# Kernel tuning notes

Measured on AMD Instinct MI355X. Metric: run time of the kernel, lower is better.

The kernel has to match this reference:

```python
import jax, jax.numpy as jnp
import numpy as np

B_, L_, D_, R_, N_ = 8, 1024, 512, 32, 16  # batch, seq(in_channels), dim(=dim_inner), dt_rank, d_state


def setup_inputs() -> dict:
    key = jax.random.key(0)
    ks = jax.random.split(key, 8)
    s = lambda k, shape, scale: jax.random.normal(k, shape, dtype=jnp.float32) * scale
    inv = D_ ** -0.5
    return {
        "x": jax.random.uniform(ks[0], (B_, L_, D_), dtype=jnp.float32),
        "W1": s(ks[1], (D_, D_), inv), "b1": jnp.zeros((D_,), jnp.float32),
        "W2": s(ks[2], (D_, D_), inv), "b2": jnp.zeros((D_,), jnp.float32),
        "Wout": s(ks[3], (D_, D_), inv), "bout": jnp.zeros((D_,), jnp.float32),
        "conv_w": s(ks[4], (L_, L_, 3), (3 * L_) ** -0.5),  # Conv1d(L_, L_, k=3) weight (O,I,W)
        "conv_b": jnp.zeros((L_,), jnp.float32),
        "W_dbc": s(ks[5], (R_ + 2 * N_, D_), inv),          # deltaBC projection (no bias)
        "W_dt": s(ks[6], (D_, R_), R_ ** -0.5),             # dt_proj weight
        "b_dt": jnp.zeros((D_,), jnp.float32),
        "A_log": jnp.log(jnp.tile(jnp.arange(1, N_ + 1, dtype=jnp.float32), (D_, 1))),  # (D, N)
        "Dp": jnp.ones((D_,), jnp.float32),
    }


def _silu(v):
    return v * jax.nn.sigmoid(v)


def _selective_scan(u, delta, A, Bm, Cm, Dp):
    # u, delta: (b, l, d); A: (d, n); Bm, Cm: (b, l, n); Dp: (d,)
    dA = jnp.exp(jnp.einsum('bld,dn->bldn', delta, A))          # (b,l,d,n)
    dBu = jnp.einsum('bld,bln,bld->bldn', delta, Bm, u)          # (b,l,d,n)

    def step(h, inp):
        dA_t, dBu_t, C_t = inp                                   # (b,d,n),(b,d,n),(b,n)
        h = dA_t * h + dBu_t
        return h, jnp.einsum('bdn,bn->bd', h, C_t)

    h0 = jnp.zeros((u.shape[0], u.shape[2], A.shape[1]), u.dtype)
    _, ys = jax.lax.scan(step, h0, (dA.transpose(1, 0, 2, 3), dBu.transpose(1, 0, 2, 3), Cm.transpose(1, 0, 2)))
    return ys.transpose(1, 0, 2) + u * Dp                        # (b,l,d)


def reference(x, W1, b1, W2, b2, Wout, bout, conv_w, conv_b, W_dbc, W_dt, b_dt, A_log, Dp):
    skip = x
    x1 = x @ W1.T + b1                                            # proj_one
    x2 = x @ W2.T + b2                                            # proj_two
    # Conv1d over channel axis = L_ (dim 1), spatial axis = D_ (dim 2)
    x1 = jax.lax.conv_general_dilated(x1, conv_w, window_strides=(1,), padding=((1, 1),),
                                      dimension_numbers=('NCW', 'OIW', 'NCW')) + conv_b[None, :, None]
    x1 = _silu(x1)
    # SSM (zeta-style): deltaBC -> split -> dt_proj -> softplus -> selective scan
    dbc = x1 @ W_dbc.T                                            # (b,l,R+2N)
    delta = jax.nn.softplus(dbc[..., :R_] @ W_dt.T + b_dt)        # (b,l,d)
    Bm, Cm = dbc[..., R_:R_ + N_], dbc[..., R_ + N_:]
    A = -jnp.exp(A_log)
    y = _selective_scan(x1, delta, A, Bm, Cm, Dp)
    out = y * _silu(x2) + skip
    return out @ Wout.T + bout
```

## Files before the change

### kernel.cpp

```cpp
#include <hip/hip_runtime.h>
#include <hip/hip_bf16.h>
#include <hip/hip_fp16.h>

typedef __hip_bfloat16 bf16;
typedef __bf16 bf16x8 __attribute__((ext_vector_type(8)));
typedef float f32x4 __attribute__((ext_vector_type(4)));

static_assert(sizeof(bf16) == 2, "bf16 must be 2 bytes");

#define NC 32
#define CH 32
#define X1TP_BSTRIDE (514L * 1024)

__device__ __forceinline__ float silu_f(float v) { return v / (1.0f + __expf(-v)); }

__device__ __forceinline__ void gload16(const bf16* g, bf16* l) {
  __builtin_amdgcn_global_load_lds((const __attribute__((address_space(1))) void*)g,
                                   (__attribute__((address_space(3))) void*)l,
                                   16, 0, 0);
}

template <int N> __device__ __forceinline__ void wait_vm() {
  static_assert(N == 0 || N == 4 || N == 6 || N == 8 || N == 12, "add case");
  if constexpr (N == 0)       asm volatile("s_waitcnt vmcnt(0)" ::: "memory");
  else if constexpr (N == 4)  asm volatile("s_waitcnt vmcnt(4)" ::: "memory");
  else if constexpr (N == 6)  asm volatile("s_waitcnt vmcnt(6)" ::: "memory");
  else if constexpr (N == 8)  asm volatile("s_waitcnt vmcnt(8)" ::: "memory");
  else if constexpr (N == 12) asm volatile("s_waitcnt vmcnt(12)" ::: "memory");
}

__global__ __launch_bounds__(256) void prep_all(
    const float* __restrict__ x, const float* __restrict__ W1,
    const float* __restrict__ W2, const float* __restrict__ Wout,
    const float* __restrict__ Wdbc, const float* __restrict__ convw,
    bf16* __restrict__ xb, bf16* __restrict__ w1b, bf16* __restrict__ w2b,
    bf16* __restrict__ woutb, bf16* __restrict__ wdbcb,
    bf16* __restrict__ cws, bf16* __restrict__ x1tp) {
  const int gid = blockIdx.x * 256 + threadIdx.x;
  auto cvt4 = [](const float* src, bf16* dst, long q) {
    float4 v = *reinterpret_cast<const float4*>(src + q * 4);
    ushort4 s;
    s.x = __builtin_bit_cast(unsigned short, __float2bfloat16(v.x));
    s.y = __builtin_bit_cast(unsigned short, __float2bfloat16(v.y));
    s.z = __builtin_bit_cast(unsigned short, __float2bfloat16(v.z));
    s.w = __builtin_bit_cast(unsigned short, __float2bfloat16(v.w));
    *reinterpret_cast<ushort4*>(dst + q * 4) = s;
  };
  if (gid < 1048576) {
    cvt4(x, xb, gid);
  } else if (gid < 1114112) {
    cvt4(W1, w1b, gid - 1048576);
  } else if (gid < 1179648) {
    cvt4(W2, w2b, gid - 1114112);
  } else if (gid < 1245184) {
    cvt4(Wout, woutb, gid - 1179648);
  } else if (gid < 1253376) {
    cvt4(Wdbc, wdbcb, gid - 1245184);
  } else if (gid < 2301952) {
    long idx = gid - 1253376;
    int o = (int)(idx >> 10), i = (int)(idx & 1023);
    float a = convw[idx * 3], b = convw[idx * 3 + 1], c = convw[idx * 3 + 2];
    cws[(long)o * 3072 + i]        = __float2bfloat16(a);
    cws[(long)o * 3072 + 1024 + i] = __float2bfloat16(b);
    cws[(long)o * 3072 + 2048 + i] = __float2bfloat16(c);
  } else {
    int e = gid - 2301952;
    int b = e >> 11, rem = e & 2047;
    int r = rem >> 10, ii = rem & 1023;
    x1tp[(long)b * X1TP_BSTRIDE + (long)r * (513 * 1024) + ii] = __float2bfloat16(0.f);
  }
}

template <int EPI, int BM, int BN, int CONVB, int NBUF>
__device__ __forceinline__ void gemm_body(const bf16* __restrict__ A,
                                          const bf16* __restrict__ Bw,
                                          const float* __restrict__ bias,
                                          float* __restrict__ outf,
                                          bf16* __restrict__ outb,
                                          int M, int N, int K, int lda, int ldb,
                                          long sAz, long sBz, long sOz,
                                          int bx, int by, int z,
                                          bf16* As, bf16* Bs) {
  constexpr int BK = 64;
  constexpr int MI = BM / 32, WNF = BN / 32;
  constexpr int APW = BM / 32, BPW = BN / 32;
  constexpr int IPW = APW + BPW;

  const int tid = threadIdx.x;
  const int w = tid >> 6, l = tid & 63;
  const int wm = w >> 1, wn = w & 1;
  const int m0 = bx * BM, n0 = by * BN;
  const bf16* Ab = A + (long)z * sAz + (long)m0 * lda;
  const bf16* Bb = Bw + (long)z * sBz;

  const int lrow = l >> 3;
  const int lcol = (((l & 7) ^ (l >> 3)) << 3);

  auto stage = [&](int buf, int k0) {
#pragma unroll
    for (int j = 0; j < APW; ++j) {
      int iss = w * APW + j;
      int row = iss * 8 + lrow;
      gload16(Ab + (long)row * lda + k0 + lcol, &As[buf * BM * 64 + iss * 512]);
    }
#pragma unroll
    for (int j = 0; j < BPW; ++j) {
      int iss = w * BPW + j;
      int row = iss * 8 + lrow;
      const bf16* src;
      if (CONVB) src = Bb + (long)(n0 + row + (k0 >> 10)) * 1024 + (k0 & 1023) + lcol;
      else       src = Bb + (long)(n0 + row) * ldb + k0 + lcol;
      gload16(src, &Bs[buf * BN * 64 + iss * 512]);
    }
  };

  f32x4 acc[MI][WNF] = {};
  const int nt = K / BK;
  const int lr = l & 15;
  const int lko = (l >> 4) * 8;
  const int xorm = (lr & 7) << 3;

#pragma unroll
  for (int s = 0; s < NBUF - 1; ++s) stage(s, s * BK);
  for (int t = 0; t < nt; ++t) {
    const int cur = t % NBUF;
    if (t + NBUF - 1 < nt) {
      stage((t + NBUF - 1) % NBUF, (t + NBUF - 1) * BK);
      wait_vm<(NBUF - 1) * IPW>();
    } else {
      wait_vm<0>();
    }
    __builtin_amdgcn_s_barrier();
    __builtin_amdgcn_sched_barrier(0);
#pragma unroll
    for (int kk = 0; kk < 2; ++kk) {
      const int col = (lko + kk * 32) ^ xorm;
      bf16x8 af[MI], bfg[WNF];
#pragma unroll
      for (int mi = 0; mi < MI; ++mi)
        af[mi] = *reinterpret_cast<const bf16x8*>(
            &As[cur * BM * 64 + (wm * (BM / 2) + mi * 16 + lr) * 64 + col]);
#pragma unroll
      for (int ni = 0; ni < WNF; ++ni)
        bfg[ni] = *reinterpret_cast<const bf16x8*>(
            &Bs[cur * BN * 64 + (wn * (BN / 2) + ni * 16 + lr) * 64 + col]);
#pragma unroll
      for (int mi = 0; mi < MI; ++mi)
#pragma unroll
        for (int ni = 0; ni < WNF; ++ni)
          acc[mi][ni] = __builtin_amdgcn_mfma_f32_16x16x32_bf16(af[mi], bfg[ni], acc[mi][ni], 0, 0, 0);
    }
    __builtin_amdgcn_sched_barrier(0);
    __builtin_amdgcn_s_barrier();
  }

  const int lq = l >> 4;
#pragma unroll
  for (int mi = 0; mi < MI; ++mi) {
#pragma unroll
    for (int ni = 0; ni < WNF; ++ni) {
#pragma unroll
      for (int j = 0; j < 4; ++j) {
        int m = m0 + wm * (BM / 2) + mi * 16 + lq * 4 + j;
        int n = n0 + wn * (BN / 2) + ni * 16 + lr;
        float v = acc[mi][ni][j];
        if (EPI == 2) {
          v += bias[m];
          (outb + (long)z * sOz)[(long)m * N + n] = __float2bfloat16(silu_f(v));
        } else if (EPI == 3) {
          outf[(long)m * N + n] = v;
        } else if (EPI == 4) {
          v += bias[n];
          outf[(long)m * N + n] = v;
        } else if (EPI == 5) {
          v += bias[m];
          int b = n >> 10, li = n & 1023;
          outb[(long)b * X1TP_BSTRIDE + (long)(m + 1) * 1024 + li] = __float2bfloat16(v);
        } else {
          v += bias[n];
          outb[(long)m * N + n] = __float2bfloat16(silu_f(v));
        }
      }
    }
  }
}

template <int EPI, int BM, int BN, int CONVB, int NBUF, int GX, int GY>
__global__ __launch_bounds__(256) void gemm_nt(const bf16* __restrict__ A,
                                               const bf16* __restrict__ Bw,
                                               const float* __restrict__ bias,
                                               float* __restrict__ outf,
                                               bf16* __restrict__ outb,
                                               int M, int N, int K, int lda, int ldb,
                                               long sAz, long sBz, long sOz) {
  __shared__ __align__(16) bf16 As[NBUF * BM * 64];
  __shared__ __align__(16) bf16 Bs[NBUF * BN * 64];
  const int bid = (blockIdx.x & 7) * ((int)gridDim.x >> 3) + (blockIdx.x >> 3);
  const int by = bid % GY;
  const int bx = (bid / GY) % GX;
  const int z  = bid / (GX * GY);
  gemm_body<EPI, BM, BN, CONVB, NBUF>(A, Bw, bias, outf, outb, M, N, K, lda, ldb,
                                      sAz, sBz, sOz, bx, by, z, As, Bs);
}

__global__ __launch_bounds__(256) void gemm_dual(
    const bf16* __restrict__ w1b, const bf16* __restrict__ xb1,
    const float* __restrict__ b1, bf16* __restrict__ x1tp,
    const bf16* __restrict__ xb2, const bf16* __restrict__ w2b,
    const float* __restrict__ b2, bf16* __restrict__ x2g) {
  __shared__ __align__(16) bf16 As[2 * 128 * 64];
  __shared__ __align__(16) bf16 Bs[2 * 128 * 64];
  int bid = (blockIdx.x & 7) * 64 + (blockIdx.x >> 3);
  if (bid < 256) {
    int by = bid & 63, bx = bid >> 6;
    gemm_body<5, 128, 128, 0, 2>(w1b, xb1, b1, nullptr, x1tp, 512, 8192, 512, 512, 512,
                                 0, 0, 0, bx, by, 0, As, Bs);
  } else {
    bid -= 256;
    int by = bid & 3, bx = bid >> 2;
    gemm_body<6, 128, 128, 0, 2>(xb2, w2b, b2, nullptr, x2g, 8192, 512, 512, 512, 512,
                                 0, 0, 0, bx, by, 0, As, Bs);
  }
}

__global__ __launch_bounds__(256) void delta_kernel(const float* __restrict__ dbc,
                                                    const float* __restrict__ W_dt,
                                                    const float* __restrict__ b_dt,
                                                    __half* __restrict__ delta) {
  const int tid = threadIdx.x;
  const int d = blockIdx.x * 256 + tid;
  const int r0 = blockIdx.y * 8;
  __shared__ float sD[8][32];
  {
    int tt = tid >> 5, j = tid & 31;
    sD[tt][j] = dbc[(long)(r0 + tt) * 64 + j];
  }
  __syncthreads();
  float wdt[32];
#pragma unroll
  for (int r = 0; r < 32; r += 4) {
    float4 v = *reinterpret_cast<const float4*>(&W_dt[(long)d * 32 + r]);
    wdt[r] = v.x; wdt[r + 1] = v.y; wdt[r + 2] = v.z; wdt[r + 3] = v.w;
  }
  const float bd = b_dt[d];
#pragma unroll
  for (int tt = 0; tt < 8; ++tt) {
    float a = bd;
#pragma unroll
    for (int r = 0; r < 32; ++r) a = fmaf(sD[tt][r], wdt[r], a);
    delta[(long)(r0 + tt) * 512 + d] = __float2half(fmaxf(a, 0.f) + log1pf(__expf(-fabsf(a))));
  }
}

__global__ __launch_bounds__(256) void scan_p1(const bf16* __restrict__ u_bf,
                                               const float* __restrict__ dbc,
                                               const __half* __restrict__ delta,
                                               const float* __restrict__ A_log,
                                               __half* __restrict__ P,
                                               __half* __restrict__ Q) {
  const int tid = threadIdx.x;
  const int nh = tid & 1;
  const int d = blockIdx.x * 128 + (tid >> 1);
  const int c = blockIdx.y, b = blockIdx.z;
  __shared__ float sB[CH][16];
  for (int i = tid; i < CH * 16; i += 256) {
    int tt = i >> 4, j = i & 15;
    sB[tt][j] = dbc[((long)b * 1024 + c * CH + tt) * 64 + 32 + j];
  }
  __syncthreads();
  float Adn[8];
#pragma unroll
  for (int n = 0; n < 8; ++n) Adn[n] = -__expf(A_log[d * 16 + nh * 8 + n]);
  float p[8], q[8];
#pragma unroll
  for (int n = 0; n < 8; ++n) { p[n] = 1.f; q[n] = 0.f; }
  const long rowb = (long)b * 1024 + c * CH;
  for (int tt = 0; tt < CH; ++tt) {
    long off = (rowb + tt) * 512 + d;
    float dv = __half2float(delta[off]);
    float uv = __bfloat162float(u_bf[off]);
    float s = dv * uv;
#pragma unroll
    for (int n = 0; n < 8; ++n) {
      float dA = __expf(dv * Adn[n]);
      p[n] *= dA;
      q[n] = fmaf(dA, q[n], s * sB[tt][nh * 8 + n]);
    }
  }
  __half* Pp = P + ((long)b * NC + c) * 8192 + (long)d * 16 + nh * 8;
  __half* Qp = Q + ((long)b * NC + c) * 8192 + (long)d * 16 + nh * 8;
  __half tp[8], tq[8];
#pragma unroll
  for (int n = 0; n < 8; ++n) { tp[n] = __float2half(p[n]); tq[n] = __float2half(q[n]); }
  *reinterpret_cast<uint4*>(Pp) = *reinterpret_cast<uint4*>(tp);
  *reinterpret_cast<uint4*>(Qp) = *reinterpret_cast<uint4*>(tq);
}

__global__ __launch_bounds__(256) void scan_p2(const __half* __restrict__ P,
                                               const __half* __restrict__ Q,
                                               __half* __restrict__ Hin) {
  const int dn = blockIdx.x * 256 + threadIdx.x;
  const int b = blockIdx.y;
  float h = 0.f;
#pragma unroll 4
  for (int c = 0; c < NC; ++c) {
    long idx = ((long)b * NC + c) * 8192 + dn;
    Hin[idx] = __float2half(h);
    h = fmaf(__half2float(P[idx]), h, __half2float(Q[idx]));
  }
}

__global__ __launch_bounds__(256) void scan_p3(const bf16* __restrict__ u_bf,
                                               const float* __restrict__ dbc,
                                               const __half* __restrict__ delta,
                                               const float* __restrict__ A_log,
                                               const float* __restrict__ Dp,
                                               const bf16* __restrict__ x2g,
                                               const bf16* __restrict__ xres,
                                               const __half* __restrict__ Hin,
                                               bf16* __restrict__ zb) {
  const int tid = threadIdx.x;
  const int nh = tid & 1;
  const int d = blockIdx.x * 128 + (tid >> 1);
  const int c = blockIdx.y, b = blockIdx.z;
  __shared__ float sBC[CH][32];
  for (int i = tid; i < CH * 32; i += 256) {
    int tt = i >> 5, j = i & 31;
    sBC[tt][j] = dbc[((long)b * 1024 + c * CH + tt) * 64 + 32 + j];
  }
  __syncthreads();
  float Adn[8];
#pragma unroll
  for (int n = 0; n < 8; ++n) Adn[n] = -__expf(A_log[d * 16 + nh * 8 + n]);
  float h[8];
  {
    const __half* Hp = Hin + ((long)b * NC + c) * 8192 + (long)d * 16 + nh * 8;
    __half th[8];
    *reinterpret_cast<uint4*>(th) = *reinterpret_cast<const uint4*>(Hp);
#pragma unroll
    for (int n = 0; n < 8; ++n) h[n] = __half2float(th[n]);
  }
  const float Dpv = Dp[d];
  const long rowb = (long)b * 1024 + c * CH;
  for (int tt = 0; tt < CH; ++tt) {
    long off = (rowb + tt) * 512 + d;
    float dv = __half2float(delta[off]);
    float uv = __bfloat162float(u_bf[off]);
    float s = dv * uv;
    float y = nh ? 0.f : uv * Dpv;
#pragma unroll
    for (int n = 0; n < 8; ++n) {
      float dA = __expf(dv * Adn[n]);
      h[n] = fmaf(dA, h[n], s * sBC[tt][nh * 8 + n]);
      y = fmaf(h[n], sBC[tt][16 + nh * 8 + n], y);
    }
    y += __shfl_xor(y, 1);
    if (nh == 0) {
      float gate = __bfloat162float(x2g[off]);
      float xv = __bfloat162float(xres[off]);
      zb[off] = __float2bfloat16(fmaf(y, gate, xv));
    }
  }
}

extern "C" void kernel_launch(void* const* d_in, const int* in_sizes, int n_in,
                              void* d_out, int out_size, void* d_ws, size_t ws_size,
                              hipStream_t stream) {
  (void)in_sizes; (void)n_in; (void)out_size; (void)ws_size;
  const float* x    = (const float*)d_in[0];
  const float* W1   = (const float*)d_in[1];
  const float* b1   = (const float*)d_in[2];
  const float* W2   = (const float*)d_in[3];
  const float* b2   = (const float*)d_in[4];
  const float* Wout = (const float*)d_in[5];
  const float* bout = (const float*)d_in[6];
  const float* convw = (const float*)d_in[7];
  const float* convb = (const float*)d_in[8];
  const float* Wdbc = (const float*)d_in[9];
  const float* Wdt  = (const float*)d_in[10];
  const float* bdt  = (const float*)d_in[11];
  const float* Alog = (const float*)d_in[12];
  const float* Dp   = (const float*)d_in[13];
  float* out = (float*)d_out;

  char* ws = (char*)d_ws;
  size_t off = 0;
  auto alloc = [&](size_t bytes) { void* p = ws + off; off += (bytes + 255) & ~(size_t)255; return p; };
  bf16* xb      = (bf16*)alloc(8192L * 512 * 2);
  bf16* w1b     = (bf16*)alloc(512L * 512 * 2);
  bf16* w2b     = (bf16*)alloc(512L * 512 * 2);
  bf16* woutb   = (bf16*)alloc(512L * 512 * 2);
  bf16* wdbcb   = (bf16*)alloc(64L * 512 * 2);
  bf16* cws     = (bf16*)alloc(1024L * 3072 * 2);
  bf16* x1tp    = (bf16*)alloc(8L * X1TP_BSTRIDE * 2);
  bf16* x2g     = (bf16*)alloc(8192L * 512 * 2);
  bf16* x1s     = (bf16*)alloc(8192L * 512 * 2);
  float* dbc    = (float*)alloc(8192L * 64 * 4);
  __half* delta = (__half*)alloc(8192L * 512 * 2);
  __half* P     = (__half*)alloc(8L * NC * 8192 * 2);
  __half* Q     = (__half*)alloc(8L * NC * 8192 * 2);
  __half* Hin   = (__half*)alloc(8L * NC * 8192 * 2);
  bf16* zb = xb;

  prep_all<<<9056, 256, 0, stream>>>(x, W1, W2, Wout, Wdbc, convw,
                                     xb, w1b, w2b, woutb, wdbcb, cws, x1tp);
  gemm_dual<<<512, 256, 0, stream>>>(w1b, xb, b1, x1tp, xb, w2b, b2, x2g);
  gemm_nt<2, 64, 128, 1, 3, 16, 4><<<512, 256, 0, stream>>>(
      cws, x1tp, convb, nullptr, x1s, 1024, 512, 3072, 3072, 0,
      0, X1TP_BSTRIDE, 1024L * 512);
  gemm_nt<3, 64, 64, 0, 3, 128, 1><<<128, 256, 0, stream>>>(
      x1s, wdbcb, nullptr, dbc, nullptr, 8192, 64, 512, 512, 512, 0, 0, 0);
  delta_kernel<<<dim3(2, 1024), 256, 0, stream>>>(dbc, Wdt, bdt, delta);
  scan_p1<<<dim3(4, NC, 8), 256, 0, stream>>>(x1s, dbc, delta, Alog, P, Q);
  scan_p2<<<dim3(32, 8, 1), 256, 0, stream>>>(P, Q, Hin);
  scan_p3<<<dim3(4, NC, 8), 256, 0, stream>>>(x1s, dbc, delta, Alog, Dp, x2g, xb, Hin, zb);
  gemm_nt<4, 64, 128, 0, 3, 128, 4><<<512, 256, 0, stream>>>(
      zb, woutb, bout, out, nullptr, 8192, 512, 512, 512, 512, 0, 0, 0);
}
```

Before: 163.9 us.

## Fuse dt projection and softplus into scan kernels, drop delta buffer

Removes the standalone delta_kernel and computes delta = softplus(dbc[:R] @ W_dt^T + b_dt) per chunk inside both scan_p1 and scan_p3, storing it in shared memory. This eliminates one kernel launch and the write and two reads of an 8 MB fp16 delta tensor. In exchange, the 32-wide dot product and softplus are computed twice, once in each scan pass, and shared memory per block grows. Delta now stays in fp32 instead of being rounded to fp16.

```diff
diff --git a/kernel.cpp b/kernel.cpp
--- a/kernel.cpp
+++ b/kernel.cpp
@@ -223,51 +223,47 @@
   }
 }
 
-__global__ __launch_bounds__(256) void delta_kernel(const float* __restrict__ dbc,
-                                                    const float* __restrict__ W_dt,
-                                                    const float* __restrict__ b_dt,
-                                                    __half* __restrict__ delta) {
-  const int tid = threadIdx.x;
-  const int d = blockIdx.x * 256 + tid;
-  const int r0 = blockIdx.y * 8;
-  __shared__ float sD[8][32];
-  {
-    int tt = tid >> 5, j = tid & 31;
-    sD[tt][j] = dbc[(long)(r0 + tt) * 64 + j];
-  }
-  __syncthreads();
-  float wdt[32];
-#pragma unroll
-  for (int r = 0; r < 32; r += 4) {
-    float4 v = *reinterpret_cast<const float4*>(&W_dt[(long)d * 32 + r]);
-    wdt[r] = v.x; wdt[r + 1] = v.y; wdt[r + 2] = v.z; wdt[r + 3] = v.w;
-  }
-  const float bd = b_dt[d];
-#pragma unroll
-  for (int tt = 0; tt < 8; ++tt) {
-    float a = bd;
-#pragma unroll
-    for (int r = 0; r < 32; ++r) a = fmaf(sD[tt][r], wdt[r], a);
-    delta[(long)(r0 + tt) * 512 + d] = __float2half(fmaxf(a, 0.f) + log1pf(__expf(-fabsf(a))));
-  }
-}
-
 __global__ __launch_bounds__(256) void scan_p1(const bf16* __restrict__ u_bf,
                                                const float* __restrict__ dbc,
-                                               const __half* __restrict__ delta,
+                                               const float* __restrict__ W_dt,
+                                               const float* __restrict__ b_dt,
                                                const float* __restrict__ A_log,
                                                __half* __restrict__ P,
                                                __half* __restrict__ Q) {
   const int tid = threadIdx.x;
+  const int c = blockIdx.y, b = blockIdx.z;
+  __shared__ float sD[CH][64];
+  __shared__ float sDel[CH][128];
+  for (int i = tid; i < CH * 16; i += 256) {
+    int tt = i >> 4, j4 = i & 15;
+    *reinterpret_cast<float4*>(&sD[tt][j4 * 4]) =
+        *reinterpret_cast<const float4*>(&dbc[((long)b * 1024 + c * CH + tt) * 64 + j4 * 4]);
+  }
+  __syncthreads();
+  {
+    const int d_loc = tid & 127, th = tid >> 7;
+    const int dg = blockIdx.x * 128 + d_loc;
+    float wdt[32];
+#pragma unroll
+    for (int r = 0; r < 32; r += 4) {
+      float4 v = *reinterpret_cast<const float4*>(&W_dt[(long)dg * 32 + r]);
+      wdt[r] = v.x; wdt[r + 1] = v.y; wdt[r + 2] = v.z; wdt[r + 3] = v.w;
+    }
+    const float bd = b_dt[dg];
+#pragma unroll
+    for (int k = 0; k < 16; ++k) {
+      int tt = th * 16 + k;
+      float a = bd;
+#pragma unroll
+      for (int r = 0; r < 32; ++r) a = fmaf(sD[tt][r], wdt[r], a);
+      sDel[tt][d_loc] = fmaxf(a, 0.f) + log1pf(__expf(-fabsf(a)));
+    }
+  }
+  __syncthreads();
+
   const int nh = tid & 1;
-  const int d = blockIdx.x * 128 + (tid >> 1);
-  const int c = blockIdx.y, b = blockIdx.z;
-  __shared__ float sB[CH][16];
-  for (int i = tid; i < CH * 16; i += 256) {
-    int tt = i >> 4, j = i & 15;
-    sB[tt][j] = dbc[((long)b * 1024 + c * CH + tt) * 64 + 32 + j];
-  }
-  __syncthreads();
+  const int dl = tid >> 1;
+  const int d = blockIdx.x * 128 + dl;
   float Adn[8];
 #pragma unroll
   for (int n = 0; n < 8; ++n) Adn[n] = -__expf(A_log[d * 16 + nh * 8 + n]);
@@ -276,15 +272,14 @@
   for (int n = 0; n < 8; ++n) { p[n] = 1.f; q[n] = 0.f; }
   const long rowb = (long)b * 1024 + c * CH;
   for (int tt = 0; tt < CH; ++tt) {
-    long off = (rowb + tt) * 512 + d;
-    float dv = __half2float(delta[off]);
-    float uv = __bfloat162float(u_bf[off]);
+    float dv = sDel[tt][dl];
+    float uv = __bfloat162float(u_bf[(rowb + tt) * 512 + d]);
     float s = dv * uv;
 #pragma unroll
     for (int n = 0; n < 8; ++n) {
       float dA = __expf(dv * Adn[n]);
       p[n] *= dA;
-      q[n] = fmaf(dA, q[n], s * sB[tt][nh * 8 + n]);
+      q[n] = fmaf(dA, q[n], s * sD[tt][32 + nh * 8 + n]);
     }
   }
   __half* Pp = P + ((long)b * NC + c) * 8192 + (long)d * 16 + nh * 8;
@@ -312,7 +307,8 @@
 
 __global__ __launch_bounds__(256) void scan_p3(const bf16* __restrict__ u_bf,
                                                const float* __restrict__ dbc,
-                                               const __half* __restrict__ delta,
+                                               const float* __restrict__ W_dt,
+                                               const float* __restrict__ b_dt,
                                                const float* __restrict__ A_log,
                                                const float* __restrict__ Dp,
                                                const bf16* __restrict__ x2g,
@@ -320,39 +316,63 @@
                                                const __half* __restrict__ Hin,
                                                bf16* __restrict__ zb) {
   const int tid = threadIdx.x;
+  const int c = blockIdx.y, b = blockIdx.z;
+  __shared__ float sD[CH][64];
+  __shared__ float sDel[CH][128];
+  for (int i = tid; i < CH * 16; i += 256) {
+    int tt = i >> 4, j4 = i & 15;
+    *reinterpret_cast<float4*>(&sD[tt][j4 * 4]) =
+        *reinterpret_cast<const float4*>(&dbc[((long)b * 1024 + c * CH + tt) * 64 + j4 * 4]);
+  }
+  __syncthreads();
+  {
+    const int d_loc = tid & 127, th = tid >> 7;
+    const int dg = blockIdx.x * 128 + d_loc;
+    float wdt[32];
+#pragma unroll
+    for (int r = 0; r < 32; r += 4) {
+      float4 v = *reinterpret_cast<const float4*>(&W_dt[(long)dg * 32 + r]);
+      wdt[r] = v.x; wdt[r + 1] = v.y; wdt[r + 2] = v.z; wdt[r + 3] = v.w;
+    }
+    const float bd = b_dt[dg];
+#pragma unroll
+    for (int k = 0; k < 16; ++k) {
+      int tt = th * 16 + k;
+      float a = bd;
+#pragma unroll
+      for (int r = 0; r < 32; ++r) a = fmaf(sD[tt][r], wdt[r], a);
+      sDel[tt][d_loc] = fmaxf(a, 0.f) + log1pf(__expf(-fabsf(a)));
+    }
+  }
+  __syncthreads();
+
   const int nh = tid & 1;
-  const int d = blockIdx.x * 128 + (tid >> 1);
-  const int c = blockIdx.y, b = blockIdx.z;
-  __shared__ float sBC[CH][32];
-  for (int i = tid; i < CH * 32; i += 256) {
-    int tt = i >> 5, j = i & 31;
-    sBC[tt][j] = dbc[((long)b * 1024 + c * CH + tt) * 64 + 32 + j];
-  }
-  __syncthreads();
+  const int dl = tid >> 1;
+  const int d = blockIdx.x * 128 + dl;
   float Adn[8];
 #pragma unroll
   for (int n = 0; n < 8; ++n) Adn[n] = -__expf(A_log[d * 16 + nh * 8 + n]);
   float h[8];
   {
     const __half* Hp = Hin + ((long)b * NC + c) * 8192 + (long)d * 16 + nh * 8;
-    __half th[8];
-    *reinterpret_cast<uint4*>(th) = *reinterpret_cast<const uint4*>(Hp);
-#pragma unroll
-    for (int n = 0; n < 8; ++n) h[n] = __half2float(th[n]);
+    __half th8[8];
+    *reinterpret_cast<uint4*>(th8) = *reinterpret_cast<const uint4*>(Hp);
+#pragma unroll
+    for (int n = 0; n < 8; ++n) h[n] = __half2float(th8[n]);
   }
   const float Dpv = Dp[d];
   const long rowb = (long)b * 1024 + c * CH;
   for (int tt = 0; tt < CH; ++tt) {
     long off = (rowb + tt) * 512 + d;
-    float dv = __half2float(delta[off]);
+    float dv = sDel[tt][dl];
     float uv = __bfloat162float(u_bf[off]);
     float s = dv * uv;
     float y = nh ? 0.f : uv * Dpv;
 #pragma unroll
     for (int n = 0; n < 8; ++n) {
       float dA = __expf(dv * Adn[n]);
-      h[n] = fmaf(dA, h[n], s * sBC[tt][nh * 8 + n]);
-      y = fmaf(h[n], sBC[tt][16 + nh * 8 + n], y);
+      h[n] = fmaf(dA, h[n], s * sD[tt][32 + nh * 8 + n]);
+      y = fmaf(h[n], sD[tt][48 + nh * 8 + n], y);
     }
     y += __shfl_xor(y, 1);
     if (nh == 0) {
@@ -396,7 +416,6 @@
   bf16* x2g     = (bf16*)alloc(8192L * 512 * 2);
   bf16* x1s     = (bf16*)alloc(8192L * 512 * 2);
   float* dbc    = (float*)alloc(8192L * 64 * 4);
-  __half* delta = (__half*)alloc(8192L * 512 * 2);
   __half* P     = (__half*)alloc(8L * NC * 8192 * 2);
   __half* Q     = (__half*)alloc(8L * NC * 8192 * 2);
   __half* Hin   = (__half*)alloc(8L * NC * 8192 * 2);
@@ -410,10 +429,9 @@
       0, X1TP_BSTRIDE, 1024L * 512);
   gemm_nt<3, 64, 64, 0, 3, 128, 1><<<128, 256, 0, stream>>>(
       x1s, wdbcb, nullptr, dbc, nullptr, 8192, 64, 512, 512, 512, 0, 0, 0);
-  delta_kernel<<<dim3(2, 1024), 256, 0, stream>>>(dbc, Wdt, bdt, delta);
-  scan_p1<<<dim3(4, NC, 8), 256, 0, stream>>>(x1s, dbc, delta, Alog, P, Q);
+  scan_p1<<<dim3(4, NC, 8), 256, 0, stream>>>(x1s, dbc, Wdt, bdt, Alog, P, Q);
   scan_p2<<<dim3(32, 8, 1), 256, 0, stream>>>(P, Q, Hin);
-  scan_p3<<<dim3(4, NC, 8), 256, 0, stream>>>(x1s, dbc, delta, Alog, Dp, x2g, xb, Hin, zb);
+  scan_p3<<<dim3(4, NC, 8), 256, 0, stream>>>(x1s, dbc, Wdt, bdt, Alog, Dp, x2g, xb, Hin, zb);
   gemm_nt<4, 64, 128, 0, 3, 128, 4><<<512, 256, 0, stream>>>(
       zb, woutb, bout, out, nullptr, 8192, 512, 512, 512, 512, 0, 0, 0);
 }
```

After: 163.0 us. Within noise of the previous version (-0.5%).
